# Kernel tuning notes

Hardware: AMD Instinct MI355X
Metric: run time of the kernel (lower is better)

The kernel has to match this reference:

```python
import jax, jax.numpy as jnp
import numpy as np

EMBED = 1024
KEY = 64
HEAD = 64
CTX = 4096
BATCH = 8


def _linear(x, w, b):
    # torch nn.Linear: y = x @ W.T + b, W shape [out, in]
    return x @ w.T + b


def setup_inputs() -> dict:
    key = jax.random.key(0)
    ks = jax.random.split(key, 11)
    s_e = 1.0 / np.sqrt(EMBED)
    s_k = 1.0 / np.sqrt(KEY)
    return {
        "embeddings": jax.random.normal(ks[0], (BATCH, CTX, EMBED), dtype=jnp.float32),
        "kw1": jax.random.uniform(ks[1], (KEY, EMBED), jnp.float32, -s_e, s_e),
        "kb1": jax.random.uniform(ks[2], (KEY,), jnp.float32, -s_e, s_e),
        "kw2": jax.random.uniform(ks[3], (KEY, KEY), jnp.float32, -s_k, s_k),
        "kb2": jax.random.uniform(ks[4], (KEY,), jnp.float32, -s_k, s_k),
        "qw1": jax.random.uniform(ks[5], (KEY, EMBED), jnp.float32, -s_e, s_e),
        "qb1": jax.random.uniform(ks[6], (KEY,), jnp.float32, -s_e, s_e),
        "qw2": jax.random.uniform(ks[7], (KEY, KEY), jnp.float32, -s_k, s_k),
        "qb2": jax.random.uniform(ks[8], (KEY,), jnp.float32, -s_k, s_k),
        "vw": jax.random.uniform(ks[9], (HEAD, EMBED), jnp.float32, -s_e, s_e),
        "vb": jax.random.uniform(ks[10], (HEAD,), jnp.float32, -s_e, s_e),
    }


def reference(embeddings, kw1, kb1, kw2, kb2, qw1, qb1, qw2, qb2, vw, vb):
    T = embeddings.shape[1]
    keys = jax.nn.relu(_linear(jax.nn.relu(_linear(embeddings, kw1, kb1)), kw2, kb2))
    queries = jax.nn.relu(_linear(jax.nn.relu(_linear(embeddings, qw1, qb1)), qw2, qb2))
    values = _linear(embeddings, vw, vb)
    # scores: [B, T, T]
    scores = jnp.einsum("btk,bsk->bts", queries, keys) / np.sqrt(KEY).astype(np.float32)
    # Faithful to original: tril(ones) * -1e10 added (masks lower triangle incl. diagonal)
    mask = jnp.tril(jnp.ones((T, T), dtype=jnp.float32)) * jnp.float32(-1e10)
    weights = jax.nn.softmax(scores + mask, axis=-1)
    return jnp.einsum("bts,bsh->bth", weights, values)
```

## Files before the change

kernel.cpp:

```cpp
#include <hip/hip_runtime.h>
#include <hip/hip_bf16.h>
#include <math.h>

#define NB   8
#define TCTX 4096
#define ED   1024
#define KD   64

typedef __attribute__((ext_vector_type(8))) short bf16x8;
typedef __attribute__((ext_vector_type(4))) float f32x4;

#define LOG2E  1.44269504088896340736f
#define SCALE2 (0.125f * LOG2E)
#define MASK2  (-1e10f * LOG2E)

__device__ __forceinline__ void lds_fence() {
    asm volatile("s_waitcnt lgkmcnt(0)" ::: "memory");
    __builtin_amdgcn_sched_barrier(0);
}

__device__ __forceinline__ unsigned short f2bf(float f) {
    union { float f; unsigned u; } c; c.f = f;
    return (unsigned short)((c.u + 0x7FFFu + ((c.u >> 16) & 1u)) >> 16);
}
__device__ __forceinline__ int swz(int row, int byteoff) {
    return row * 128 + (byteoff ^ ((row & 7) << 4));
}
__device__ __forceinline__ f32x4 fzero4() {
    f32x4 z; z[0] = 0.f; z[1] = 0.f; z[2] = 0.f; z[3] = 0.f; return z;
}
__device__ __forceinline__ void gl_lds16(const void* g, void* l) {
    __builtin_amdgcn_global_load_lds(
        (const __attribute__((address_space(1))) unsigned int*)g,
        (__attribute__((address_space(3))) unsigned int*)l, 16, 0, 0);
}
__device__ __forceinline__ unsigned cvtpk_bf16(float lo, float hi) {
    unsigned r;
    asm("v_cvt_pk_bf16_f32 %0, %1, %2" : "=v"(r) : "v"(lo), "v"(hi));
    return r;
}

__global__ __launch_bounds__(256) void prep_kernel(
    const float* __restrict__ kw1, const float* __restrict__ qw1,
    const float* __restrict__ vw,  const float* __restrict__ kw2,
    const float* __restrict__ qw2,
    unsigned short* __restrict__ W1p, unsigned short* __restrict__ W2p)
{
    int idx = blockIdx.x * 256 + threadIdx.x;
    if (idx < 24576) {
        int ks = idx / 1536, rem = idx % 1536;
        int r = rem >> 3, bb = rem & 7;
        int c = bb ^ (r & 7);
        const float* src = (r < 64)  ? (kw1 + r * ED)
                         : (r < 128) ? (qw1 + (r - 64) * ED)
                                     : (vw  + (r - 128) * ED);
        src += ks * 64 + c * 8;
        unsigned short* dst = W1p + (size_t)idx * 8;
        #pragma unroll
        for (int e = 0; e < 8; ++e) dst[e] = f2bf(src[e]);
    } else if (idx < 25600) {
        int j = idx - 24576;
        int lane = j & 63, kh = (j >> 6) & 1, n = (j >> 7) & 3, kq = j >> 9;
        int row = n * 16 + (lane & 15);
        int ko  = kh * 32 + (lane >> 4) * 8;
        const float* src = (kq ? qw2 : kw2) + row * 64 + ko;
        unsigned short* dst = W2p + (size_t)j * 8;
        #pragma unroll
        for (int e = 0; e < 8; ++e) dst[e] = f2bf(src[e]);
    }
}

__global__ __launch_bounds__(256, 2) void proj_kernel(
    const float* __restrict__ emb,
    const unsigned short* __restrict__ W1p, const unsigned short* __restrict__ W2p,
    const float* __restrict__ kb1, const float* __restrict__ kb2,
    const float* __restrict__ qb1, const float* __restrict__ qb2,
    const float* __restrict__ vb,
    unsigned short* __restrict__ Qo, unsigned short* __restrict__ Ko,
    unsigned short* __restrict__ Vt)
{
    __shared__ __align__(16) char lds[80 * 1024];

    const int tid  = threadIdx.x;
    const int lane = tid & 63;
    const int w    = tid >> 6;
    const int lr   = lane & 15;
    const int lg   = lane >> 4;
    const long r0  = (long)blockIdx.x * 64;
    const int  b   = blockIdx.x >> 6;
    const int  tb  = (blockIdx.x & 63) * 64;

    const float* embB = emb + r0 * ED;

    f32x4 acc[12];
    #pragma unroll
    for (int j = 0; j < 12; ++j) acc[j] = fzero4();

    auto stageA = [&](int buf, int ks) {
        char* Abuf = lds + buf * 16 * 1024;
        const float* eb = embB + ks * 64;
        #pragma unroll
        for (int j = 0; j < 4; ++j) {
            int chunk = j * 4 + w;
            int r = chunk * 4 + (lane >> 4);
            int c = (lane & 15) ^ (r & 7);
            gl_lds16(eb + (long)r * ED + c * 4, Abuf + chunk * 1024);
        }
    };
    auto stageB = [&](int buf, int ks) {
        char* Bbuf = lds + 32 * 1024 + buf * 24 * 1024;
        const unsigned short* wb = W1p + (size_t)ks * 12288;
        #pragma unroll
        for (int j = 0; j < 6; ++j) {
            int chunk = j * 4 + w;
            gl_lds16(wb + chunk * 512 + lane * 8, Bbuf + chunk * 1024);
        }
    };

    stageA(0, 0); stageB(0, 0);
    __syncthreads();

    int cur = 0;
    for (int ks = 0; ks < 16; ++ks) {
        if (ks < 15) { stageA(cur ^ 1, ks + 1); stageB(cur ^ 1, ks + 1); }
        char* Ac = lds + cur * 16 * 1024;
        char* Bc = lds + 32 * 1024 + cur * 24 * 1024;
        const int r = w * 16 + lr;
        #pragma unroll
        for (int kh = 0; kh < 2; ++kh) {
            int cb0 = kh * 8 + lg * 2;
            float4 fa = *(const float4*)(Ac + r * 256 + ((cb0 ^ (r & 7)) * 16));
            float4 fb = *(const float4*)(Ac + r * 256 + (((cb0 + 1) ^ (r & 7)) * 16));
            bf16x8 a;
            a[0] = (short)f2bf(fa.x); a[1] = (short)f2bf(fa.y);
            a[2] = (short)f2bf(fa.z); a[3] = (short)f2bf(fa.w);
            a[4] = (short)f2bf(fb.x); a[5] = (short)f2bf(fb.y);
            a[6] = (short)f2bf(fb.z); a[7] = (short)f2bf(fb.w);
            #pragma unroll
            for (int n = 0; n < 12; ++n) {
                bf16x8 bv = *(const bf16x8*)(Bc + swz(n * 16 + lr, kh * 64 + lg * 16));
                acc[n] = __builtin_amdgcn_mfma_f32_16x16x32_bf16(a, bv, acc[n], 0, 0, 0);
            }
        }
        __syncthreads();
        cur ^= 1;
    }

    char* H  = lds + w * 2048;
    char* VT = lds + 16 * 1024;

    #pragma unroll
    for (int kq = 0; kq < 2; ++kq) {
        const float* b1 = kq ? qb1 : kb1;
        const float* b2 = kq ? qb2 : kb2;
        unsigned short* dst = kq ? Qo : Ko;
        const float oscale = kq ? SCALE2 : 1.0f;
        #pragma unroll
        for (int n = 0; n < 4; ++n) {
            int col = n * 16 + lr;
            float bias = b1[col];
            #pragma unroll
            for (int rr = 0; rr < 4; ++rr) {
                int row = lg * 4 + rr;
                *(unsigned short*)(H + swz(row, col * 2)) =
                    f2bf(fmaxf(acc[kq * 4 + n][rr] + bias, 0.f));
            }
        }
        lds_fence();
        bf16x8 a2k0 = *(const bf16x8*)(H + swz(lr, 0 * 64 + lg * 16));
        bf16x8 a2k1 = *(const bf16x8*)(H + swz(lr, 1 * 64 + lg * 16));
        lds_fence();

        f32x4 acc2[4];
        #pragma unroll
        for (int n = 0; n < 4; ++n) acc2[n] = fzero4();
        #pragma unroll
        for (int n = 0; n < 4; ++n) {
            bf16x8 w2f0 = *(const bf16x8*)(W2p + ((kq * 4 + n) * 2 + 0) * 512 + lane * 8);
            bf16x8 w2f1 = *(const bf16x8*)(W2p + ((kq * 4 + n) * 2 + 1) * 512 + lane * 8);
            acc2[n] = __builtin_amdgcn_mfma_f32_16x16x32_bf16(a2k0, w2f0, acc2[n], 0, 0, 0);
            acc2[n] = __builtin_amdgcn_mfma_f32_16x16x32_bf16(a2k1, w2f1, acc2[n], 0, 0, 0);
        }
        #pragma unroll
        for (int n = 0; n < 4; ++n) {
            int col = n * 16 + lr;
            float bias = b2[col];
            #pragma unroll
            for (int rr = 0; rr < 4; ++rr) {
                long rg = r0 + w * 16 + lg * 4 + rr;
                dst[rg * KD + col] = f2bf(fmaxf(acc2[n][rr] + bias, 0.f) * oscale);
            }
        }
    }

    #pragma unroll
    for (int n = 0; n < 4; ++n) {
        int col = n * 16 + lr;
        float bias = vb[col];
        #pragma unroll
        for (int rr = 0; rr < 4; ++rr) {
            int tl = w * 16 + lg * 4 + rr;
            *(unsigned short*)(VT + swz(col, tl * 2)) = f2bf(acc[8 + n][rr] + bias);
        }
    }
    __syncthreads();
    #pragma unroll
    for (int it = 0; it < 2; ++it) {
        int c = it * 256 + tid;
        int h = c >> 3, c4 = c & 7;
        *(int4*)(Vt + ((long)b * KD + h) * TCTX + tb + c4 * 8) =
            *(const int4*)(VT + swz(h, c4 * 16));
    }
}

__global__ __launch_bounds__(128) void attn_kernel(
    const unsigned short* __restrict__ Qb,
    const unsigned short* __restrict__ Kb,
    const unsigned short* __restrict__ Vt,
    float* __restrict__ Opart, float2* __restrict__ MSum)
{
    __shared__ __align__(16) char lds[20 * 1024];

    const int bid  = blockIdx.x;
    const int half = bid & 1;
    const int rest = bid >> 1;
    const int b    = rest & 7;
    const int qr   = rest >> 3;
    const int qi   = (qr + 127) & 127;
    const int t0   = qi * 32;
    const int tid = threadIdx.x, lane = tid & 63, w = tid >> 6;
    const int lr  = lane & 15, lg = lane >> 4;
    const int tg  = t0 + w * 16 + lr;

    char* Kl = lds;
    char* Vl = lds + 8 * 1024;
    char* QP = lds + 16 * 1024 + w * 2048;

    const unsigned short* Qg  = Qb + ((long)b * TCTX + t0 + w * 16) * KD;
    const unsigned short* Kg0 = Kb + (long)b * TCTX * KD;
    const unsigned short* Vg0 = Vt + (long)b * KD * TCTX;

    const int srow = lane >> 3;
    const int sblk = lane & 7;

    const int s0q = (qi == 127) ? 0 : (qi >> 1);
    const int len = 64 - s0q;
    const int mid = s0q + ((len + 1) >> 1);
    const int s_lo = half ? mid : s0q;
    const int s_hi = half ? 64  : mid;

    auto stageKV = [&](int si) {
        const unsigned short* Kg = Kg0 + si * 64 * KD;
        const unsigned short* Vg = Vg0 + si * 64;
        #pragma unroll
        for (int j = 0; j < 4; ++j) {
            int chunk = w * 4 + j;
            int r = chunk * 8 + srow;
            int c = sblk ^ (r & 7);
            gl_lds16(Kg + r * KD + c * 8, Kl + chunk * 1024);
            gl_lds16(Vg + (long)r * TCTX + c * 8, Vl + chunk * 1024);
        }
    };

    float m2 = MASK2, sum_p = 0.f;
    f32x4 O[4];
    #pragma unroll
    for (int n = 0; n < 4; ++n) O[n] = fzero4();

    if (s_lo < s_hi) {
        #pragma unroll
        for (int j = 0; j < 2; ++j) {
            int r = j * 8 + srow;
            int c = sblk ^ (r & 7);
            gl_lds16(Qg + r * KD + c * 8, QP + j * 1024);
        }
        stageKV(s_lo);
        __syncthreads();

        bf16x8 qf[2];
        #pragma unroll
        for (int kh = 0; kh < 2; ++kh)
            qf[kh] = *(const bf16x8*)(QP + swz(lr, kh * 64 + lg * 16));

        for (int si = s_lo; si < s_hi; ++si) {
            f32x4 sc[4];
            #pragma unroll
            for (int mi = 0; mi < 4; ++mi) sc[mi] = fzero4();
            __builtin_amdgcn_s_setprio(1);
            #pragma unroll
            for (int kh = 0; kh < 2; ++kh) {
                #pragma unroll
                for (int mi = 0; mi < 4; ++mi) {
                    bf16x8 kf = *(const bf16x8*)(Kl + swz(mi * 16 + lr, kh * 64 + lg * 16));
                    sc[mi] = __builtin_amdgcn_mfma_f32_16x16x32_bf16(kf, qf[kh], sc[mi], 0, 0, 0);
                }
            }
            __builtin_amdgcn_s_setprio(0);

            const int thr = tg - si * 64;
            float s2v[4][4];
            #pragma unroll
            for (int mi = 0; mi < 4; ++mi)
                #pragma unroll
                for (int rr = 0; rr < 4; ++rr) {
                    int sl = mi * 16 + lg * 4 + rr;
                    s2v[mi][rr] = (sl <= thr) ? MASK2 : sc[mi][rr];
                }

            float pml = s2v[0][0];
            #pragma unroll
            for (int mi = 0; mi < 4; ++mi)
                #pragma unroll
                for (int rr = 0; rr < 4; ++rr) pml = fmaxf(pml, s2v[mi][rr]);

            if (!__all(pml - m2 <= 8.0f)) {
                float pm = pml;
                pm = fmaxf(pm, __shfl_xor(pm, 16, 64));
                pm = fmaxf(pm, __shfl_xor(pm, 32, 64));
                float mnew = fmaxf(m2, pm);
                float scl = __builtin_amdgcn_exp2f(m2 - mnew);
                m2 = mnew;
                sum_p *= scl;
                #pragma unroll
                for (int rr = 0; rr < 4; ++rr) {
                    float sb = __shfl(scl, lg * 4 + rr, 64);
                    #pragma unroll
                    for (int n = 0; n < 4; ++n) O[n][rr] *= sb;
                }
            }
            float ls = 0.f;
            #pragma unroll
            for (int mi = 0; mi < 4; ++mi)
                #pragma unroll
                for (int rr = 0; rr < 4; ++rr) {
                    s2v[mi][rr] = __builtin_amdgcn_exp2f(s2v[mi][rr] - m2);
                    ls += s2v[mi][rr];
                }
            sum_p += ls;

            #pragma unroll
            for (int mi = 0; mi < 4; ++mi) {
                unsigned lo = cvtpk_bf16(s2v[mi][0], s2v[mi][1]);
                unsigned hi = cvtpk_bf16(s2v[mi][2], s2v[mi][3]);
                *(uint2*)(QP + swz(lr, mi * 32 + lg * 8)) = make_uint2(lo, hi);
            }
            lds_fence();
            bf16x8 ap0 = *(const bf16x8*)(QP + swz(lr, 0 * 64 + lg * 16));
            bf16x8 ap1 = *(const bf16x8*)(QP + swz(lr, 1 * 64 + lg * 16));
            lds_fence();

            __builtin_amdgcn_s_setprio(1);
            #pragma unroll
            for (int n = 0; n < 4; ++n) {
                bf16x8 bv0 = *(const bf16x8*)(Vl + swz(n * 16 + lr, 0 * 64 + lg * 16));
                bf16x8 bv1 = *(const bf16x8*)(Vl + swz(n * 16 + lr, 1 * 64 + lg * 16));
                O[n] = __builtin_amdgcn_mfma_f32_16x16x32_bf16(ap0, bv0, O[n], 0, 0, 0);
                O[n] = __builtin_amdgcn_mfma_f32_16x16x32_bf16(ap1, bv1, O[n], 0, 0, 0);
            }
            __builtin_amdgcn_s_setprio(0);

            __syncthreads();
            if (si + 1 < s_hi) {
                stageKV(si + 1);
                __syncthreads();
            }
        }
    }

    float sr = sum_p;
    sr += __shfl_xor(sr, 16, 64);
    sr += __shfl_xor(sr, 32, 64);
    const long rbase = (long)b * TCTX + t0 + w * 16;
    #pragma unroll
    for (int rr = 0; rr < 4; ++rr) {
        int tl = lg * 4 + rr;
        long rowi = (rbase + tl) * 2 + half;
        #pragma unroll
        for (int n = 0; n < 4; ++n)
            Opart[rowi * 64 + n * 16 + lr] = O[n][rr];
    }
    if (lg == 0)
        MSum[(rbase + lr) * 2 + half] = make_float2(m2, sr);
}

__global__ __launch_bounds__(64) void combine_kernel(
    const float* __restrict__ Opart, const float2* __restrict__ MSum,
    float* __restrict__ out)
{
    const int lane = threadIdx.x;
    const long r0 = (long)blockIdx.x * 64;
    for (int i = 0; i < 64; ++i) {
        long r = r0 + i;
        float2 A = MSum[r * 2 + 0];
        float2 B = MSum[r * 2 + 1];
        float M  = fmaxf(A.x, B.x);
        float wa = __builtin_amdgcn_exp2f(A.x - M);
        float wb = __builtin_amdgcn_exp2f(B.x - M);
        float denom = A.y * wa + B.y * wb;
        float oa = Opart[(r * 2 + 0) * 64 + lane];
        float ob = Opart[(r * 2 + 1) * 64 + lane];
        out[r * 64 + lane] = (oa * wa + ob * wb) / denom;
    }
}

extern "C" void kernel_launch(void* const* d_in, const int* in_sizes, int n_in,
                              void* d_out, int out_size, void* d_ws, size_t ws_size,
                              hipStream_t stream) {
    const float* emb = (const float*)d_in[0];
    const float* kw1 = (const float*)d_in[1];
    const float* kb1 = (const float*)d_in[2];
    const float* kw2 = (const float*)d_in[3];
    const float* kb2 = (const float*)d_in[4];
    const float* qw1 = (const float*)d_in[5];
    const float* qb1 = (const float*)d_in[6];
    const float* qw2 = (const float*)d_in[7];
    const float* qb2 = (const float*)d_in[8];
    const float* vw  = (const float*)d_in[9];
    const float* vb  = (const float*)d_in[10];

    unsigned short* Qb  = (unsigned short*)d_ws;
    unsigned short* Kb  = Qb + (size_t)NB * TCTX * KD;
    unsigned short* Vt  = Kb + (size_t)NB * TCTX * KD;
    unsigned short* W1p = Vt + (size_t)NB * TCTX * KD;
    unsigned short* W2p = W1p + 196608;
    float*  Opart = (float*)(W2p + 8192);
    float2* MSum  = (float2*)(Opart + (size_t)NB * TCTX * 2 * KD);

    hipLaunchKernelGGL(prep_kernel, dim3(100), dim3(256), 0, stream,
                       kw1, qw1, vw, kw2, qw2, W1p, W2p);
    hipLaunchKernelGGL(proj_kernel, dim3(512), dim3(256), 0, stream,
                       emb, W1p, W2p, kb1, kb2, qb1, qb2, vb,
                       Qb, Kb, Vt);
    hipLaunchKernelGGL(attn_kernel, dim3(2048), dim3(128), 0, stream,
                       Qb, Kb, Vt, Opart, MSum);
    hipLaunchKernelGGL(combine_kernel, dim3(512), dim3(64), 0, stream,
                       Opart, MSum, (float*)d_out);
}
```

Before: 96.89 us.

## Split K/V staging to overlap loads with compute; widen combine kernel grid

Staging of K and V tiles is split, so the next K tile is prefetched right after the QK MFMAs and the next V tile after the PV MFMAs. This overlaps global-to-LDS copies with the softmax and PV work and drops the extra barrier that used to follow staging. The combine kernel becomes a grid-stride loop with 256-thread blocks and a larger grid, which should improve occupancy for that memory-bound pass. Prefetch correctness now relies on the remaining barriers ordering each tile's reads before it is overwritten, and the number of barriers per iteration stays about the same.

```diff
diff --git a/kernel.cpp b/kernel.cpp
--- a/kernel.cpp
+++ b/kernel.cpp
@@ -249,15 +249,23 @@
     const int s_lo = half ? mid : s0q;
     const int s_hi = half ? 64  : mid;
 
-    auto stageKV = [&](int si) {
+    auto stageK = [&](int si) {
         const unsigned short* Kg = Kg0 + si * 64 * KD;
-        const unsigned short* Vg = Vg0 + si * 64;
         #pragma unroll
         for (int j = 0; j < 4; ++j) {
             int chunk = w * 4 + j;
             int r = chunk * 8 + srow;
             int c = sblk ^ (r & 7);
             gl_lds16(Kg + r * KD + c * 8, Kl + chunk * 1024);
+        }
+    };
+    auto stageV = [&](int si) {
+        const unsigned short* Vg = Vg0 + si * 64;
+        #pragma unroll
+        for (int j = 0; j < 4; ++j) {
+            int chunk = w * 4 + j;
+            int r = chunk * 8 + srow;
+            int c = sblk ^ (r & 7);
             gl_lds16(Vg + (long)r * TCTX + c * 8, Vl + chunk * 1024);
         }
     };
@@ -274,7 +282,8 @@
             int c = sblk ^ (r & 7);
             gl_lds16(Qg + r * KD + c * 8, QP + j * 1024);
         }
-        stageKV(s_lo);
+        stageK(s_lo);
+        stageV(s_lo);
         __syncthreads();
 
         bf16x8 qf[2];
@@ -296,6 +305,9 @@
                 }
             }
             __builtin_amdgcn_s_setprio(0);
+
+            __syncthreads();
+            if (si + 1 < s_hi) stageK(si + 1);
 
             const int thr = tg - si * 64;
             float s2v[4][4];
@@ -360,10 +372,7 @@
             __builtin_amdgcn_s_setprio(0);
 
             __syncthreads();
-            if (si + 1 < s_hi) {
-                stageKV(si + 1);
-                __syncthreads();
-            }
+            if (si + 1 < s_hi) stageV(si + 1);
         }
     }
 
@@ -383,23 +392,24 @@
         MSum[(rbase + lr) * 2 + half] = make_float2(m2, sr);
 }
 
-__global__ __launch_bounds__(64) void combine_kernel(
+__global__ __launch_bounds__(256) void combine_kernel(
     const float* __restrict__ Opart, const float2* __restrict__ MSum,
     float* __restrict__ out)
 {
-    const int lane = threadIdx.x;
-    const long r0 = (long)blockIdx.x * 64;
-    for (int i = 0; i < 64; ++i) {
-        long r = r0 + i;
+    const long total = (long)NB * TCTX * KD;
+    for (long idx = (long)blockIdx.x * 256 + threadIdx.x; idx < total;
+         idx += (long)gridDim.x * 256) {
+        long r = idx >> 6;
+        int  h = (int)(idx & 63);
         float2 A = MSum[r * 2 + 0];
         float2 B = MSum[r * 2 + 1];
         float M  = fmaxf(A.x, B.x);
         float wa = __builtin_amdgcn_exp2f(A.x - M);
         float wb = __builtin_amdgcn_exp2f(B.x - M);
         float denom = A.y * wa + B.y * wb;
-        float oa = Opart[(r * 2 + 0) * 64 + lane];
-        float ob = Opart[(r * 2 + 1) * 64 + lane];
-        out[r * 64 + lane] = (oa * wa + ob * wb) / denom;
+        float oa = Opart[(r * 2 + 0) * 64 + h];
+        float ob = Opart[(r * 2 + 1) * 64 + h];
+        out[idx] = (oa * wa + ob * wb) / denom;
     }
 }
 
@@ -433,6 +443,6 @@
                        Qb, Kb, Vt);
     hipLaunchKernelGGL(attn_kernel, dim3(2048), dim3(128), 0, stream,
                        Qb, Kb, Vt, Opart, MSum);
-    hipLaunchKernelGGL(combine_kernel, dim3(512), dim3(64), 0, stream,
+    hipLaunchKernelGGL(combine_kernel, dim3(2048), dim3(256), 0, stream,
                        Opart, MSum, (float*)d_out);
 }
```

Result: faster. 85.40 us (-11.9%).
